# Kernel optimization log

Measured on AMD Instinct MI355X. Metric: run time of the kernel, lower is better.

Reference implementation:

```python
import jax, jax.numpy as jnp
import numpy as np

B = 131072      # batch
G = 8           # number of groups
GS = 8          # features per group (n_features = G*GS = 64)
K = 8           # n_basis
O = 16          # kan_out_dim
TOT = G * O     # 128, GroupKANLayer output dim
R = 10          # n_rules
FIN = 20        # fuzzy_in_dim = max(2*n_rules, 8)
EPS_BN = 1e-5


def setup_inputs() -> dict:
    key = jax.random.key(0)
    ks = jax.random.split(key, 8)
    x = jax.random.normal(ks[0], (B, G * GS), dtype=jnp.float32)
    # per-group GaussianRBF params (one shared RBF per group, applied to each feature)
    rbf_centres = jnp.tile(jnp.linspace(-3.0, 3.0, K, dtype=jnp.float32)[None, :], (G, 1))
    rbf_log_widths = jnp.zeros((G, K), dtype=jnp.float32)
    rbf_weights = jax.random.normal(ks[1], (G, K), dtype=jnp.float32) * 0.1
    rbf_linear_w = jnp.ones((G,), dtype=jnp.float32)
    # group projections: kaiming normal fan_in (relu gain sqrt(2))
    proj_W = jax.random.normal(ks[2], (G, O, GS), dtype=jnp.float32) * np.sqrt(2.0 / GS)
    proj_b = jnp.zeros((G, O), dtype=jnp.float32)
    bn1_gamma = jnp.ones((TOT,), dtype=jnp.float32)
    bn1_beta = jnp.zeros((TOT,), dtype=jnp.float32)
    # fuzzy_proj linear (xavier uniform) TOT -> FIN
    a = np.sqrt(6.0 / (TOT + FIN))
    fp_W = jax.random.uniform(ks[3], (FIN, TOT), dtype=jnp.float32, minval=-a, maxval=a)
    fp_b = jnp.zeros((FIN,), dtype=jnp.float32)
    bn2_gamma = jnp.ones((FIN,), dtype=jnp.float32)
    bn2_beta = jnp.zeros((FIN,), dtype=jnp.float32)
    # IT2 fuzzy layer params
    fz_centres = jax.random.uniform(ks[4], (R, FIN), dtype=jnp.float32, minval=-1.0, maxval=1.0)
    fz_log_su = jnp.full((R, FIN), -0.7, dtype=jnp.float32)
    fz_log_sl = jnp.full((R, FIN), -1.2, dtype=jnp.float32)
    # sparse rule head
    head_W = jax.random.normal(ks[5], (1, R), dtype=jnp.float32) * 0.05
    head_b = jnp.zeros((1,), dtype=jnp.float32)
    return {
        'x': x, 'rbf_centres': rbf_centres, 'rbf_log_widths': rbf_log_widths,
        'rbf_weights': rbf_weights, 'rbf_linear_w': rbf_linear_w,
        'proj_W': proj_W, 'proj_b': proj_b,
        'bn1_gamma': bn1_gamma, 'bn1_beta': bn1_beta,
        'fp_W': fp_W, 'fp_b': fp_b, 'bn2_gamma': bn2_gamma, 'bn2_beta': bn2_beta,
        'fz_centres': fz_centres, 'fz_log_su': fz_log_su, 'fz_log_sl': fz_log_sl,
        'head_W': head_W, 'head_b': head_b,
    }


def _batchnorm(h, gamma, beta):
    # training-mode BatchNorm1d: normalize with batch mean / biased variance
    mu = h.mean(axis=0)
    var = h.var(axis=0)
    return (h - mu) * jax.lax.rsqrt(var + EPS_BN) * gamma + beta


def _forward(x, rbf_centres, rbf_log_widths, rbf_weights, rbf_linear_w,
             proj_W, proj_b, bn1_gamma, bn1_beta, fp_W, fp_b,
             bn2_gamma, bn2_beta, fz_centres, fz_log_su, fz_log_sl,
             head_W, head_b):
    b = x.shape[0]
    xg = x.reshape(b, G, GS)                               # groups are contiguous index slices
    sigma = jnp.exp(rbf_log_widths) + 1e-6                 # [G,K]
    # Gaussian RBF over all groups/features at once: [B,G,GS,K]
    rbf = jnp.exp(-0.5 * ((xg[..., None] - rbf_centres[:, None, :]) / sigma[:, None, :]) ** 2)
    act = rbf_linear_w[None, :, None] * xg + jnp.einsum('bgfk,gk->bgf', rbf, rbf_weights)
    proj = jnp.einsum('bgf,gof->bgo', act, proj_W) + proj_b  # grouped linear, [B,G,O]
    h = _batchnorm(proj.reshape(b, TOT), bn1_gamma, bn1_beta)
    # fuzzy_proj: Linear -> BN -> GELU (torch default GELU = exact erf form)
    z = _batchnorm(h @ fp_W.T + fp_b, bn2_gamma, bn2_beta)
    z = jax.nn.gelu(z, approximate=False)                    # [B,FIN]
    # IT2 fuzzy memberships
    su = jnp.exp(fz_log_su) + 1e-6                           # [R,FIN]
    sl = jnp.minimum(jnp.exp(fz_log_sl) + 1e-6, su * 0.9)
    diff = z[:, None, :] - fz_centres[None]                  # [B,R,FIN]
    upper = jnp.exp(-0.5 * (diff / su[None]) ** 2).mean(-1)  # [B,R]
    lower = jnp.exp(-0.5 * (diff / sl[None]) ** 2).mean(-1)
    firing = 0.5 * (upper + lower)
    return firing @ head_W.T + head_b                        # [B,1]


def reference(x, rbf_centres, rbf_log_widths, rbf_weights, rbf_linear_w,
              proj_W, proj_b, bn1_gamma, bn1_beta, fp_W, fp_b,
              bn2_gamma, bn2_beta, fz_centres, fz_log_su, fz_log_sl,
              head_W, head_b):
    return _forward(x, rbf_centres, rbf_log_widths, rbf_weights, rbf_linear_w,
                    proj_W, proj_b, bn1_gamma, bn1_beta, fp_W, fp_b,
                    bn2_gamma, bn2_beta, fz_centres, fz_log_su, fz_log_sl,
                    head_W, head_b)
```

## Files before the change

kernel.cpp:

```cpp
#include <hip/hip_runtime.h>
#include <math.h>

#define B_N 131072
#define R_N 10
#define FIN_N 20

#define WS_STAT1 0
#define ST1_SZ   (64 * 352)
#define WS_MT    22528
#define WS_C     23808
#define WS_STAT2 23840
#define WS_NH    26400
#define WS_ACT   26816
#define WS_Z2    26816
#define WS_ZFULL (26816 + (size_t)64 * B_N)

__global__ __launch_bounds__(256) void k_act_moments(
    const float* __restrict__ x, const float* __restrict__ cen,
    const float* __restrict__ lw, const float* __restrict__ rw,
    const float* __restrict__ linw, float* __restrict__ act_out,
    float* __restrict__ stat1, int store)
{
    __shared__ float sAcc[4][8][44];

    const int t = threadIdx.x;
    const int g = t & 7;
    const int rl = t >> 3;

    float c_[8], nh_[8], w_[8];
#pragma unroll
    for (int k = 0; k < 8; ++k) {
        c_[k] = cen[g * 8 + k];
        float s = expf(lw[g * 8 + k]) + 1e-6f;
        nh_[k] = -0.5f / (s * s);
        w_[k] = rw[g * 8 + k];
    }
    const float lin = linw[g];

    float sumA[8], P[36];
#pragma unroll
    for (int f = 0; f < 8; ++f) sumA[f] = 0.0f;
#pragma unroll
    for (int i = 0; i < 36; ++i) P[i] = 0.0f;

    for (int row = blockIdx.x * 32 + rl; row < B_N; row += gridDim.x * 32) {
        const float* xr = x + (size_t)row * 64 + g * 8;
        float4 v0 = *(const float4*)(xr);
        float4 v1 = *(const float4*)(xr + 4);
        float xv[8] = {v0.x, v0.y, v0.z, v0.w, v1.x, v1.y, v1.z, v1.w};
        float act[8];
#pragma unroll
        for (int f = 0; f < 8; ++f) {
            float v = xv[f];
            float a = lin * v;
#pragma unroll
            for (int k = 0; k < 8; ++k) {
                float d = v - c_[k];
                a += w_[k] * __expf(d * d * nh_[k]);
            }
            act[f] = a;
        }
        if (store) {
            float* ar = act_out + (size_t)row * 64 + g * 8;
            *(float4*)(ar)     = make_float4(act[0], act[1], act[2], act[3]);
            *(float4*)(ar + 4) = make_float4(act[4], act[5], act[6], act[7]);
        }
        int idx = 0;
#pragma unroll
        for (int f = 0; f < 8; ++f) {
            sumA[f] += act[f];
#pragma unroll
            for (int f2 = 0; f2 <= f; ++f2) { P[idx] += act[f] * act[f2]; ++idx; }
        }
    }

#pragma unroll
    for (int off = 32; off >= 8; off >>= 1) {
#pragma unroll
        for (int f = 0; f < 8; ++f) sumA[f] += __shfl_down(sumA[f], off, 64);
#pragma unroll
        for (int i = 0; i < 36; ++i) P[i] += __shfl_down(P[i], off, 64);
    }
    const int wave = t >> 6, lane = t & 63;
    if (lane < 8) {
        float* dst = &sAcc[wave][lane][0];
#pragma unroll
        for (int f = 0; f < 8; ++f) dst[f] = sumA[f];
#pragma unroll
        for (int i = 0; i < 36; ++i) dst[8 + i] = P[i];
    }
    __syncthreads();
    for (int i = t; i < 352; i += 256) {
        int gg = i / 44, v = i % 44;
        float s = sAcc[0][gg][v] + sAcc[1][gg][v] + sAcc[2][gg][v] + sAcc[3][gg][v];
        atomicAdd(&stat1[(blockIdx.x & 63) * 352 + i], s);
    }
}

__global__ __launch_bounds__(256) void k_build(
    const float* __restrict__ stat1, const float* __restrict__ fpW,
    const float* __restrict__ fpb, const float* __restrict__ g1,
    const float* __restrict__ b1, const float* __restrict__ Wp,
    const float* __restrict__ pb, const float* __restrict__ lsu,
    const float* __restrict__ lsl,
    float* __restrict__ Mt, float* __restrict__ Cc, float* __restrict__ nh,
    float* __restrict__ stat2)
{
    __shared__ float Am[8][8];
    __shared__ float Sg[8][36];
    __shared__ float a_[128], bb_[128];
    const int t = threadIdx.x;

    for (int i = t; i < 352; i += 256) {
        float s = 0.0f;
        for (int st = 0; st < 64; ++st) s += stat1[st * 352 + i];
        float m = s * (1.0f / B_N);
        int g = i / 44, v = i % 44;
        if (v < 8) Am[g][v] = m; else Sg[g][v - 8] = m;
    }
    __syncthreads();

    if (t < 128) {
        const int g = t >> 4;
        float wv[8];
#pragma unroll
        for (int f = 0; f < 8; ++f) wv[f] = Wp[t * 8 + f];
        float dot = 0.0f;
#pragma unroll
        for (int f = 0; f < 8; ++f) dot += wv[f] * Am[g][f];
        const float pbv = pb[t];
        const float mu = pbv + dot;
        float e2 = pbv * pbv + 2.0f * pbv * dot;
        int idx = 0;
#pragma unroll
        for (int f = 0; f < 8; ++f)
#pragma unroll
            for (int f2 = 0; f2 <= f; ++f2) {
                float c2 = (f2 == f) ? 1.0f : 2.0f;
                e2 += c2 * wv[f] * wv[f2] * Sg[g][idx]; ++idx;
            }
        const float var = e2 - mu * mu;
        const float a = g1[t] * rsqrtf(var + 1e-5f);
        a_[t] = a;
        bb_[t] = b1[t] - mu * a;
    }
    __syncthreads();

    for (int i = t; i < 1280; i += 256) {
        int gf = i / 20, j = i % 20;
        int g = gf >> 3, f = gf & 7;
        float m = 0.0f;
        for (int o = 0; o < 16; ++o) {
            int c = g * 16 + o;
            m += fpW[j * 128 + c] * a_[c] * Wp[c * 8 + f];
        }
        Mt[i] = m;
    }
    if (t < 20) {
        float cj = fpb[t];
        for (int c = 0; c < 128; ++c)
            cj += fpW[t * 128 + c] * (a_[c] * pb[c] + bb_[c]);
        Cc[t] = cj;
    }
    for (int i = t; i < 200; i += 256) {
        float su = expf(lsu[i]) + 1e-6f;
        float sl = fminf(expf(lsl[i]) + 1e-6f, 0.9f * su);
        nh[i] = -0.5f / (su * su);
        nh[200 + i] = -0.5f / (sl * sl);
    }
    for (int i = t; i < 2560; i += 256) stat2[i] = 0.0f;
}

__global__ __launch_bounds__(128) void k_z_from_act(
    const float* __restrict__ act, const float* __restrict__ Mt,
    const float* __restrict__ Cc, float* __restrict__ zout,
    float* __restrict__ stat2)
{
    __shared__ __align__(16) float sMt[1280];
    __shared__ float sC[20];
    __shared__ float sRed[2][40];

    const int t = threadIdx.x;
    for (int i = t; i < 1280; i += 128) sMt[i] = Mt[i];
    if (t < 20) sC[t] = Cc[t];
    __syncthreads();

    const int r0 = (blockIdx.x * 128 + t) * 4;
    float zp[4][20];
#pragma unroll
    for (int r = 0; r < 4; ++r)
#pragma unroll
        for (int j = 0; j < 20; ++j) zp[r][j] = sC[j];

#pragma unroll 1
    for (int g = 0; g < 8; ++g) {
        float a[4][8];
#pragma unroll
        for (int r = 0; r < 4; ++r) {
            const float* ar = act + (size_t)(r0 + r) * 64 + g * 8;
            float4 v0 = *(const float4*)(ar);
            float4 v1 = *(const float4*)(ar + 4);
            a[r][0] = v0.x; a[r][1] = v0.y; a[r][2] = v0.z; a[r][3] = v0.w;
            a[r][4] = v1.x; a[r][5] = v1.y; a[r][6] = v1.z; a[r][7] = v1.w;
        }
#pragma unroll
        for (int f = 0; f < 8; ++f) {
            const float4* m4 = (const float4*)(sMt + (g * 8 + f) * 20);
            float4 ma = m4[0], mb = m4[1], mc = m4[2], md = m4[3], me = m4[4];
#pragma unroll
            for (int r = 0; r < 4; ++r) {
                float av = a[r][f];
                zp[r][0] += av * ma.x; zp[r][1] += av * ma.y; zp[r][2] += av * ma.z; zp[r][3] += av * ma.w;
                zp[r][4] += av * mb.x; zp[r][5] += av * mb.y; zp[r][6] += av * mb.z; zp[r][7] += av * mb.w;
                zp[r][8] += av * mc.x; zp[r][9] += av * mc.y; zp[r][10] += av * mc.z; zp[r][11] += av * mc.w;
                zp[r][12] += av * md.x; zp[r][13] += av * md.y; zp[r][14] += av * md.z; zp[r][15] += av * md.w;
                zp[r][16] += av * me.x; zp[r][17] += av * me.y; zp[r][18] += av * me.z; zp[r][19] += av * me.w;
            }
        }
    }

#pragma unroll
    for (int j = 0; j < 20; ++j) {
        *(float4*)(zout + (size_t)j * B_N + r0) =
            make_float4(zp[0][j], zp[1][j], zp[2][j], zp[3][j]);
    }

    float s_[20], q_[20];
#pragma unroll
    for (int j = 0; j < 20; ++j) {
        float s = zp[0][j] + zp[1][j] + zp[2][j] + zp[3][j];
        float q = zp[0][j]*zp[0][j] + zp[1][j]*zp[1][j] + zp[2][j]*zp[2][j] + zp[3][j]*zp[3][j];
        s_[j] = s; q_[j] = q;
    }
#pragma unroll
    for (int off = 32; off >= 1; off >>= 1) {
#pragma unroll
        for (int j = 0; j < 20; ++j) {
            s_[j] += __shfl_down(s_[j], off, 64);
            q_[j] += __shfl_down(q_[j], off, 64);
        }
    }
    const int wave = t >> 6, lane = t & 63;
    if (lane == 0) {
#pragma unroll
        for (int j = 0; j < 20; ++j) {
            sRed[wave][j] = s_[j];
            sRed[wave][20 + j] = q_[j];
        }
    }
    __syncthreads();
    if (t < 40) {
        float v = sRed[0][t] + sRed[1][t];
        atomicAdd(&stat2[(blockIdx.x & 63) * 40 + t], v);
    }
}

__device__ __forceinline__ void zpre_row(
    const float* __restrict__ xr, const float4* __restrict__ sRbf,
    const float* __restrict__ sLin, const float* __restrict__ sMt,
    const float* __restrict__ sC, float zp[20])
{
#pragma unroll
    for (int j = 0; j < 20; ++j) zp[j] = sC[j];
#pragma unroll 1
    for (int g = 0; g < 8; ++g) {
        float4 v0 = *(const float4*)(xr + g * 8);
        float4 v1 = *(const float4*)(xr + g * 8 + 4);
        float xv[8] = {v0.x, v0.y, v0.z, v0.w, v1.x, v1.y, v1.z, v1.w};
        float act[8];
        float lin = sLin[g];
#pragma unroll
        for (int f = 0; f < 8; ++f) act[f] = lin * xv[f];
#pragma unroll 1
        for (int k = 0; k < 8; ++k) {
            float4 p = sRbf[g * 8 + k];
#pragma unroll
            for (int f = 0; f < 8; ++f) {
                float d = xv[f] - p.x;
                act[f] += p.y * __expf(d * d * p.z);
            }
        }
#pragma unroll 1
        for (int f = 0; f < 8; ++f) {
            float av = act[f];
            const float4* m4 = (const float4*)(sMt + (g * 8 + f) * 20);
            float4 ma = m4[0], mb = m4[1], mc = m4[2], md = m4[3], me = m4[4];
            zp[0] += av * ma.x; zp[1] += av * ma.y; zp[2] += av * ma.z; zp[3] += av * ma.w;
            zp[4] += av * mb.x; zp[5] += av * mb.y; zp[6] += av * mb.z; zp[7] += av * mb.w;
            zp[8] += av * mc.x; zp[9] += av * mc.y; zp[10] += av * mc.z; zp[11] += av * mc.w;
            zp[12] += av * md.x; zp[13] += av * md.y; zp[14] += av * md.z; zp[15] += av * md.w;
            zp[16] += av * me.x; zp[17] += av * me.y; zp[18] += av * me.z; zp[19] += av * me.w;
        }
    }
}

__device__ __forceinline__ void load_rbf_lds(
    const float* cen, const float* lw, const float* rw, const float* linw,
    const float* Mt, const float* Cc,
    float4* sRbf, float* sLin, float* sMt, float* sC, int t)
{
    if (t < 64) {
        float s = expf(lw[t]) + 1e-6f;
        sRbf[t] = make_float4(cen[t], rw[t], -0.5f / (s * s), 0.0f);
    }
    if (t < 8)  sLin[t] = linw[t];
    if (t < 20) sC[t] = Cc[t];
    for (int i = t; i < 1280; i += 256) sMt[i] = Mt[i];
}

__global__ __launch_bounds__(256) void k_zpre_stats(
    const float* __restrict__ x, const float* __restrict__ cen,
    const float* __restrict__ lw, const float* __restrict__ rw,
    const float* __restrict__ linw, const float* __restrict__ Mt,
    const float* __restrict__ Cc, float* __restrict__ zout,
    float* __restrict__ stat2, int store)
{
    __shared__ __align__(16) float4 sRbf[64];
    __shared__ float sLin[8], sC[20];
    __shared__ __align__(16) float sMt[1280];
    __shared__ float sRed[4][40];

    const int t = threadIdx.x;
    load_rbf_lds(cen, lw, rw, linw, Mt, Cc, sRbf, sLin, sMt, sC, t);
    __syncthreads();

    const int row = blockIdx.x * 256 + t;
    float zp[20];
    zpre_row(x + (size_t)row * 64, sRbf, sLin, sMt, sC, zp);
    if (store) {
#pragma unroll
        for (int j = 0; j < 20; ++j) zout[(size_t)j * B_N + row] = zp[j];
    }
    float s_[20], q_[20];
#pragma unroll
    for (int j = 0; j < 20; ++j) { s_[j] = zp[j]; q_[j] = zp[j] * zp[j]; }
#pragma unroll
    for (int off = 32; off >= 1; off >>= 1) {
#pragma unroll
        for (int j = 0; j < 20; ++j) {
            s_[j] += __shfl_down(s_[j], off, 64);
            q_[j] += __shfl_down(q_[j], off, 64);
        }
    }
    const int wave = t >> 6, lane = t & 63;
    if (lane == 0) {
#pragma unroll
        for (int j = 0; j < 20; ++j) { sRed[wave][j] = s_[j]; sRed[wave][20 + j] = q_[j]; }
    }
    __syncthreads();
    if (t < 40) {
        float v = sRed[0][t] + sRed[1][t] + sRed[2][t] + sRed[3][t];
        atomicAdd(&stat2[(blockIdx.x & 63) * 40 + t], v);
    }
}

__device__ __forceinline__ float gelu_exact(float v) {
    return 0.5f * v * (1.0f + erff(v * 0.70710678118654752440f));
}

__device__ __forceinline__ void bn2_inline(
    const float* stat2, const float* g2, const float* b2,
    float* sT, float* sSc, float* sSh, int t)
{
    if (t < 40) {
        float s = 0.0f;
        for (int st = 0; st < 64; ++st) s += stat2[st * 40 + t];
        sT[t] = s;
    }
    __syncthreads();
    if (t < 20) {
        float mu = sT[t] * (1.0f / B_N);
        float var = sT[20 + t] * (1.0f / B_N) - mu * mu;
        float sc = g2[t] * rsqrtf(var + 1e-5f);
        sSc[t] = sc;
        sSh[t] = b2[t] - mu * sc;
    }
}

__global__ __launch_bounds__(256) void k_out2(
    const float* __restrict__ zin, const float* __restrict__ stat2,
    const float* __restrict__ g2, const float* __restrict__ b2,
    const float* __restrict__ nh, const float* __restrict__ fzc,
    const float* __restrict__ hW, const float* __restrict__ hb,
    float* __restrict__ out)
{
    __shared__ float sT[40], sSc[20], sSh[20], sHW[10];
    __shared__ __align__(16) float4 sFz[200];
    const int t = threadIdx.x;
    if (t < 10) sHW[t] = hW[t];
    for (int i = t; i < 200; i += 256)
        sFz[i] = make_float4(fzc[i], nh[i], nh[200 + i], 0.0f);
    bn2_inline(stat2, g2, b2, sT, sSc, sSh, t);
    __syncthreads();

    const int r0 = (blockIdx.x * 256 + t) * 2;
    float z0[20], z1[20];
#pragma unroll
    for (int j = 0; j < 20; ++j) {
        float2 v = *(const float2*)(zin + (size_t)j * B_N + r0);
        z0[j] = gelu_exact(sSc[j] * v.x + sSh[j]);
        z1[j] = gelu_exact(sSc[j] * v.y + sSh[j]);
    }
    const float hbv = hb[0];
    float acc0 = hbv, acc1 = hbv;
#pragma unroll 1
    for (int r = 0; r < 10; ++r) {
        float u0 = 0.0f, l0 = 0.0f, u1 = 0.0f, l1 = 0.0f;
#pragma unroll
        for (int j = 0; j < 20; ++j) {
            float4 p = sFz[r * 20 + j];
            float d0 = z0[j] - p.x, d1 = z1[j] - p.x;
            float dd0 = d0 * d0, dd1 = d1 * d1;
            u0 += __expf(dd0 * p.y); l0 += __expf(dd0 * p.z);
            u1 += __expf(dd1 * p.y); l1 += __expf(dd1 * p.z);
        }
        float w = sHW[r] * 0.025f;
        acc0 += w * (u0 + l0);
        acc1 += w * (u1 + l1);
    }
    *(float2*)(out + r0) = make_float2(acc0, acc1);
}

__global__ __launch_bounds__(256) void k_out_rec(
    const float* __restrict__ x, const float* __restrict__ cen,
    const float* __restrict__ lw, const float* __restrict__ rw,
    const float* __restrict__ linw, const float* __restrict__ Mt,
    const float* __restrict__ Cc, const float* __restrict__ stat2,
    const float* __restrict__ g2, const float* __restrict__ b2,
    const float* __restrict__ nh, const float* __restrict__ fzc,
    const float* __restrict__ hW, const float* __restrict__ hb,
    float* __restrict__ out)
{
    __shared__ __align__(16) float4 sRbf[64];
    __shared__ float sLin[8], sC[20];
    __shared__ __align__(16) float sMt[1280];
    __shared__ float sT[40], sSc[20], sSh[20], sHW[10];
    __shared__ __align__(16) float4 sFz[200];

    const int t = threadIdx.x;
    load_rbf_lds(cen, lw, rw, linw, Mt, Cc, sRbf, sLin, sMt, sC, t);
    if (t < 10) sHW[t] = hW[t];
    for (int i = t; i < 200; i += 256)
        sFz[i] = make_float4(fzc[i], nh[i], nh[200 + i], 0.0f);
    bn2_inline(stat2, g2, b2, sT, sSc, sSh, t);
    __syncthreads();

    const int row = blockIdx.x * 256 + t;
    float zp[20];
    zpre_row(x + (size_t)row * 64, sRbf, sLin, sMt, sC, zp);
    float z[20];
#pragma unroll
    for (int j = 0; j < 20; ++j)
        z[j] = gelu_exact(sSc[j] * zp[j] + sSh[j]);
    float acc = hb[0];
#pragma unroll 1
    for (int r = 0; r < 10; ++r) {
        float u = 0.0f, l = 0.0f;
#pragma unroll
        for (int j = 0; j < 20; ++j) {
            float4 p = sFz[r * 20 + j];
            float d = z[j] - p.x;
            float dd = d * d;
            u += __expf(dd * p.y);
            l += __expf(dd * p.z);
        }
        acc += sHW[r] * 0.025f * (u + l);
    }
    out[row] = acc;
}

extern "C" void kernel_launch(void* const* d_in, const int* in_sizes, int n_in,
                              void* d_out, int out_size, void* d_ws, size_t ws_size,
                              hipStream_t stream) {
    const float* x    = (const float*)d_in[0];
    const float* cen  = (const float*)d_in[1];
    const float* lw   = (const float*)d_in[2];
    const float* rw   = (const float*)d_in[3];
    const float* linw = (const float*)d_in[4];
    const float* Wp   = (const float*)d_in[5];
    const float* pb   = (const float*)d_in[6];
    const float* g1   = (const float*)d_in[7];
    const float* b1   = (const float*)d_in[8];
    const float* fpW  = (const float*)d_in[9];
    const float* fpb  = (const float*)d_in[10];
    const float* g2   = (const float*)d_in[11];
    const float* b2   = (const float*)d_in[12];
    const float* fzc  = (const float*)d_in[13];
    const float* lsu  = (const float*)d_in[14];
    const float* lsl  = (const float*)d_in[15];
    const float* hW   = (const float*)d_in[16];
    const float* hb   = (const float*)d_in[17];

    float* ws    = (float*)d_ws;
    float* stat1 = ws + WS_STAT1;
    float* Mt    = ws + WS_MT;
    float* Cc    = ws + WS_C;
    float* stat2 = ws + WS_STAT2;
    float* nh    = ws + WS_NH;
    float* actb  = ws + WS_ACT;
    float* outp  = (float*)d_out;

    const size_t needFull = (WS_ZFULL + (size_t)20 * B_N) * sizeof(float);
    const size_t needZ    = ((size_t)WS_Z2 + (size_t)20 * B_N) * sizeof(float);
    int mode = (ws_size >= needFull) ? 2 : (ws_size >= needZ ? 1 : 0);
    float* zbuf = (mode == 2) ? (ws + WS_ZFULL) : (ws + WS_Z2);

    hipMemsetAsync(stat1, 0, (size_t)ST1_SZ * sizeof(float), stream);
    k_act_moments<<<1024, 256, 0, stream>>>(x, cen, lw, rw, linw, actb, stat1,
                                            mode == 2 ? 1 : 0);
    k_build<<<1, 256, 0, stream>>>(stat1, fpW, fpb, g1, b1, Wp, pb, lsu, lsl,
                                   Mt, Cc, nh, stat2);
    if (mode == 2) {
        k_z_from_act<<<256, 128, 0, stream>>>(actb, Mt, Cc, zbuf, stat2);
        k_out2<<<256, 256, 0, stream>>>(zbuf, stat2, g2, b2, nh, fzc, hW, hb, outp);
    } else if (mode == 1) {
        k_zpre_stats<<<512, 256, 0, stream>>>(x, cen, lw, rw, linw, Mt, Cc,
                                              zbuf, stat2, 1);
        k_out2<<<256, 256, 0, stream>>>(zbuf, stat2, g2, b2, nh, fzc, hW, hb, outp);
    } else {
        k_zpre_stats<<<512, 256, 0, stream>>>(x, cen, lw, rw, linw, Mt, Cc,
                                              nullptr, stat2, 0);
        k_out_rec<<<512, 256, 0, stream>>>(x, cen, lw, rw, linw, Mt, Cc,
                                           stat2, g2, b2, nh, fzc, hW, hb, outp);
    }
}
```

Baseline: 188.5 us.

## Fuse whole pipeline into one cooperative kernel with grid syncs

Result: slower. 388.0 us (+105.9%).

```diff
diff --git a/kernel.cpp b/kernel.cpp
--- a/kernel.cpp
+++ b/kernel.cpp
@@ -1,9 +1,17 @@
 #include <hip/hip_runtime.h>
+#include <hip/hip_cooperative_groups.h>
 #include <math.h>
 
+namespace cg = cooperative_groups;
+
 #define B_N 131072
-#define R_N 10
-#define FIN_N 20
+#define CB 256
+#define CT 256
+
+#define CW_P1   0
+#define CW_MOM  (256 * 352)
+#define CW_P2   (CW_MOM + 352)
+#define CW_BN2  (CW_P2 + 256 * 40)
 
 #define WS_STAT1 0
 #define ST1_SZ   (64 * 352)
@@ -11,22 +19,307 @@
 #define WS_C     23808
 #define WS_STAT2 23840
 #define WS_NH    26400
-#define WS_ACT   26816
 #define WS_Z2    26816
-#define WS_ZFULL (26816 + (size_t)64 * B_N)
+
+__device__ __forceinline__ float gelu_exact(float v) {
+    return 0.5f * v * (1.0f + erff(v * 0.70710678118654752440f));
+}
+
+__global__ __launch_bounds__(256, 1) void k_fused(
+    const float* __restrict__ x, const float* __restrict__ cen,
+    const float* __restrict__ lw, const float* __restrict__ rw,
+    const float* __restrict__ linw, const float* __restrict__ Wp,
+    const float* __restrict__ pb, const float* __restrict__ g1,
+    const float* __restrict__ b1, const float* __restrict__ fpW,
+    const float* __restrict__ fpb, const float* __restrict__ g2,
+    const float* __restrict__ b2, const float* __restrict__ fzc,
+    const float* __restrict__ lsu, const float* __restrict__ lsl,
+    const float* __restrict__ hW, const float* __restrict__ hb,
+    float* __restrict__ ws, float* __restrict__ out)
+{
+    __shared__ float sAcc[4][8][44];
+    __shared__ __align__(16) float4 sRbf[64];
+    __shared__ float sLin[8];
+    __shared__ __align__(16) float sMt[1280];
+    __shared__ float sC[20], a_[128], bb_[128];
+    __shared__ __align__(16) float4 sFz[200];
+    __shared__ float sHW[10], sT[40], sSc[20], sSh[20];
+    __shared__ float sRed[4][40];
+
+    cg::grid_group grid = cg::this_grid();
+    const int t = threadIdx.x;
+    const int b = blockIdx.x;
+    float* part1 = ws + CW_P1;
+    float* mom   = ws + CW_MOM;
+    float* part2 = ws + CW_P2;
+    float* bn2s  = ws + CW_BN2;
+
+    {
+        const int g = t & 7, rl = t >> 3;
+        float c_[8], nh_[8], w_[8];
+#pragma unroll
+        for (int k = 0; k < 8; ++k) {
+            c_[k] = cen[g * 8 + k];
+            float s = expf(lw[g * 8 + k]) + 1e-6f;
+            nh_[k] = -0.5f / (s * s);
+            w_[k] = rw[g * 8 + k];
+        }
+        const float lin = linw[g];
+        float sumA[8], P[36];
+#pragma unroll
+        for (int f = 0; f < 8; ++f) sumA[f] = 0.0f;
+#pragma unroll
+        for (int i = 0; i < 36; ++i) P[i] = 0.0f;
+
+        for (int row = b * 32 + rl; row < B_N; row += CB * 32) {
+            const float* xr = x + (size_t)row * 64 + g * 8;
+            float4 v0 = *(const float4*)(xr);
+            float4 v1 = *(const float4*)(xr + 4);
+            float xv[8] = {v0.x, v0.y, v0.z, v0.w, v1.x, v1.y, v1.z, v1.w};
+            float act[8];
+#pragma unroll
+            for (int f = 0; f < 8; ++f) {
+                float v = xv[f];
+                float a = lin * v;
+#pragma unroll
+                for (int k = 0; k < 8; ++k) {
+                    float d = v - c_[k];
+                    a += w_[k] * __expf(d * d * nh_[k]);
+                }
+                act[f] = a;
+            }
+            int idx = 0;
+#pragma unroll
+            for (int f = 0; f < 8; ++f) {
+                sumA[f] += act[f];
+#pragma unroll
+                for (int f2 = 0; f2 <= f; ++f2) { P[idx] += act[f] * act[f2]; ++idx; }
+            }
+        }
+#pragma unroll
+        for (int off = 32; off >= 8; off >>= 1) {
+#pragma unroll
+            for (int f = 0; f < 8; ++f) sumA[f] += __shfl_down(sumA[f], off, 64);
+#pragma unroll
+            for (int i = 0; i < 36; ++i) P[i] += __shfl_down(P[i], off, 64);
+        }
+        const int wave = t >> 6, lane = t & 63;
+        if (lane < 8) {
+            float* dst = &sAcc[wave][lane][0];
+#pragma unroll
+            for (int f = 0; f < 8; ++f) dst[f] = sumA[f];
+#pragma unroll
+            for (int i = 0; i < 36; ++i) dst[8 + i] = P[i];
+        }
+        __syncthreads();
+        for (int i = t; i < 352; i += 256) {
+            int gg = i / 44, v = i % 44;
+            part1[b * 352 + i] =
+                sAcc[0][gg][v] + sAcc[1][gg][v] + sAcc[2][gg][v] + sAcc[3][gg][v];
+        }
+    }
+    __threadfence();
+    grid.sync();
+
+    for (int v = b; v < 352; v += CB) {
+        float val = part1[(size_t)t * 352 + v];
+#pragma unroll
+        for (int off = 32; off >= 1; off >>= 1) val += __shfl_down(val, off, 64);
+        if ((t & 63) == 0) sT[t >> 6] = val;
+        __syncthreads();
+        if (t == 0)
+            mom[v] = (sT[0] + sT[1] + sT[2] + sT[3]) * (1.0f / B_N);
+        __syncthreads();
+    }
+    __threadfence();
+    grid.sync();
+
+    if (t < 128) {
+        const int g = t >> 4;
+        float wv[8], Amg[8];
+#pragma unroll
+        for (int f = 0; f < 8; ++f) { wv[f] = Wp[t * 8 + f]; Amg[f] = mom[g * 44 + f]; }
+        float dot = 0.0f;
+#pragma unroll
+        for (int f = 0; f < 8; ++f) dot += wv[f] * Amg[f];
+        const float pbv = pb[t];
+        const float mu = pbv + dot;
+        float e2 = pbv * pbv + 2.0f * pbv * dot;
+        int idx = 0;
+#pragma unroll
+        for (int f = 0; f < 8; ++f)
+#pragma unroll
+            for (int f2 = 0; f2 <= f; ++f2) {
+                float c2 = (f2 == f) ? 1.0f : 2.0f;
+                e2 += c2 * wv[f] * wv[f2] * mom[g * 44 + 8 + idx]; ++idx;
+            }
+        const float var = fmaxf(e2 - mu * mu, 0.0f);
+        const float a = g1[t] * rsqrtf(var + 1e-5f);
+        a_[t] = a;
+        bb_[t] = b1[t] - mu * a;
+    }
+    if (t < 64) {
+        float s = expf(lw[t]) + 1e-6f;
+        sRbf[t] = make_float4(cen[t], rw[t], -0.5f / (s * s), 0.0f);
+    }
+    if (t < 8)  sLin[t] = linw[t];
+    if (t < 10) sHW[t] = hW[t];
+    for (int i = t; i < 200; i += 256) {
+        float su = expf(lsu[i]) + 1e-6f;
+        float sl = fminf(expf(lsl[i]) + 1e-6f, 0.9f * su);
+        sFz[i] = make_float4(fzc[i], -0.5f / (su * su), -0.5f / (sl * sl), 0.0f);
+    }
+    __syncthreads();
+    for (int i = t; i < 1280; i += 256) {
+        int gf = i / 20, j = i % 20;
+        int g = gf >> 3, f = gf & 7;
+        float m = 0.0f;
+        for (int o = 0; o < 16; ++o) {
+            int c = g * 16 + o;
+            m += fpW[j * 128 + c] * a_[c] * Wp[c * 8 + f];
+        }
+        sMt[i] = m;
+    }
+    if (t < 20) {
+        float cj = fpb[t];
+        for (int c = 0; c < 128; ++c)
+            cj += fpW[t * 128 + c] * (a_[c] * pb[c] + bb_[c]);
+        sC[t] = cj;
+    }
+    __syncthreads();
+
+    const int r0 = (b * CT + t) * 2;
+    float z[2][20];
+#pragma unroll
+    for (int j = 0; j < 20; ++j) { z[0][j] = sC[j]; z[1][j] = sC[j]; }
+    {
+        const float* xr = x + (size_t)r0 * 64;
+#pragma unroll 1
+        for (int g = 0; g < 8; ++g) {
+            float4 p0 = *(const float4*)(xr + g * 8);
+            float4 p1 = *(const float4*)(xr + g * 8 + 4);
+            float4 q0 = *(const float4*)(xr + 64 + g * 8);
+            float4 q1 = *(const float4*)(xr + 64 + g * 8 + 4);
+            float xv[2][8] = {{p0.x, p0.y, p0.z, p0.w, p1.x, p1.y, p1.z, p1.w},
+                              {q0.x, q0.y, q0.z, q0.w, q1.x, q1.y, q1.z, q1.w}};
+            float act[2][8];
+            float lin = sLin[g];
+#pragma unroll
+            for (int r = 0; r < 2; ++r)
+#pragma unroll
+                for (int f = 0; f < 8; ++f) act[r][f] = lin * xv[r][f];
+#pragma unroll 1
+            for (int k = 0; k < 8; ++k) {
+                float4 p = sRbf[g * 8 + k];
+#pragma unroll
+                for (int r = 0; r < 2; ++r)
+#pragma unroll
+                    for (int f = 0; f < 8; ++f) {
+                        float d = xv[r][f] - p.x;
+                        act[r][f] += p.y * __expf(d * d * p.z);
+                    }
+            }
+#pragma unroll 1
+            for (int f = 0; f < 8; ++f) {
+                const float4* m4 = (const float4*)(sMt + (g * 8 + f) * 20);
+                float4 ma = m4[0], mb = m4[1], mc = m4[2], md = m4[3], me = m4[4];
+#pragma unroll
+                for (int r = 0; r < 2; ++r) {
+                    float av = act[r][f];
+                    z[r][0] += av * ma.x; z[r][1] += av * ma.y; z[r][2] += av * ma.z; z[r][3] += av * ma.w;
+                    z[r][4] += av * mb.x; z[r][5] += av * mb.y; z[r][6] += av * mb.z; z[r][7] += av * mb.w;
+                    z[r][8] += av * mc.x; z[r][9] += av * mc.y; z[r][10] += av * mc.z; z[r][11] += av * mc.w;
+                    z[r][12] += av * md.x; z[r][13] += av * md.y; z[r][14] += av * md.z; z[r][15] += av * md.w;
+                    z[r][16] += av * me.x; z[r][17] += av * me.y; z[r][18] += av * me.z; z[r][19] += av * me.w;
+                }
+            }
+        }
+    }
+    {
+        float s_[20], q_[20];
+#pragma unroll
+        for (int j = 0; j < 20; ++j) {
+            s_[j] = z[0][j] + z[1][j];
+            q_[j] = z[0][j] * z[0][j] + z[1][j] * z[1][j];
+        }
+#pragma unroll
+        for (int off = 32; off >= 1; off >>= 1) {
+#pragma unroll
+            for (int j = 0; j < 20; ++j) {
+                s_[j] += __shfl_down(s_[j], off, 64);
+                q_[j] += __shfl_down(q_[j], off, 64);
+            }
+        }
+        const int wave = t >> 6, lane = t & 63;
+        if (lane == 0) {
+#pragma unroll
+            for (int j = 0; j < 20; ++j) {
+                sRed[wave][j] = s_[j];
+                sRed[wave][20 + j] = q_[j];
+            }
+        }
+        __syncthreads();
+        if (t < 40)
+            part2[b * 40 + t] = sRed[0][t] + sRed[1][t] + sRed[2][t] + sRed[3][t];
+    }
+    __threadfence();
+    grid.sync();
+
+    if (b < 40) {
+        float val = part2[(size_t)t * 40 + b];
+#pragma unroll
+        for (int off = 32; off >= 1; off >>= 1) val += __shfl_down(val, off, 64);
+        if ((t & 63) == 0) sT[t >> 6] = val;
+        __syncthreads();
+        if (t == 0) bn2s[b] = sT[0] + sT[1] + sT[2] + sT[3];
+    }
+    __threadfence();
+    grid.sync();
+
+    if (t < 40) sT[t] = bn2s[t];
+    __syncthreads();
+    if (t < 20) {
+        float mu = sT[t] * (1.0f / B_N);
+        float var = fmaxf(sT[20 + t] * (1.0f / B_N) - mu * mu, 0.0f);
+        float sc = g2[t] * rsqrtf(var + 1e-5f);
+        sSc[t] = sc;
+        sSh[t] = b2[t] - mu * sc;
+    }
+    __syncthreads();
+#pragma unroll
+    for (int r = 0; r < 2; ++r)
+#pragma unroll
+        for (int j = 0; j < 20; ++j)
+            z[r][j] = gelu_exact(sSc[j] * z[r][j] + sSh[j]);
+    const float hbv = hb[0];
+    float acc0 = hbv, acc1 = hbv;
+#pragma unroll 1
+    for (int r = 0; r < 10; ++r) {
+        float u0 = 0.0f, l0 = 0.0f, u1 = 0.0f, l1 = 0.0f;
+#pragma unroll
+        for (int j = 0; j < 20; ++j) {
+            float4 p = sFz[r * 20 + j];
+            float d0 = z[0][j] - p.x, d1 = z[1][j] - p.x;
+            float dd0 = d0 * d0, dd1 = d1 * d1;
+            u0 += __expf(dd0 * p.y); l0 += __expf(dd0 * p.z);
+            u1 += __expf(dd1 * p.y); l1 += __expf(dd1 * p.z);
+        }
+        float w = sHW[r] * 0.025f;
+        acc0 += w * (u0 + l0);
+        acc1 += w * (u1 + l1);
+    }
+    *(float2*)(out + r0) = make_float2(acc0, acc1);
+}
 
 __global__ __launch_bounds__(256) void k_act_moments(
     const float* __restrict__ x, const float* __restrict__ cen,
     const float* __restrict__ lw, const float* __restrict__ rw,
-    const float* __restrict__ linw, float* __restrict__ act_out,
-    float* __restrict__ stat1, int store)
+    const float* __restrict__ linw, float* __restrict__ stat1)
 {
     __shared__ float sAcc[4][8][44];
-
     const int t = threadIdx.x;
     const int g = t & 7;
     const int rl = t >> 3;
-
     float c_[8], nh_[8], w_[8];
 #pragma unroll
     for (int k = 0; k < 8; ++k) {
@@ -36,13 +329,11 @@
         w_[k] = rw[g * 8 + k];
     }
     const float lin = linw[g];
-
     float sumA[8], P[36];
 #pragma unroll
     for (int f = 0; f < 8; ++f) sumA[f] = 0.0f;
 #pragma unroll
     for (int i = 0; i < 36; ++i) P[i] = 0.0f;
-
     for (int row = blockIdx.x * 32 + rl; row < B_N; row += gridDim.x * 32) {
         const float* xr = x + (size_t)row * 64 + g * 8;
         float4 v0 = *(const float4*)(xr);
@@ -60,11 +351,6 @@
             }
             act[f] = a;
         }
-        if (store) {
-            float* ar = act_out + (size_t)row * 64 + g * 8;
-            *(float4*)(ar)     = make_float4(act[0], act[1], act[2], act[3]);
-            *(float4*)(ar + 4) = make_float4(act[4], act[5], act[6], act[7]);
-        }
         int idx = 0;
 #pragma unroll
         for (int f = 0; f < 8; ++f) {
@@ -73,7 +359,6 @@
             for (int f2 = 0; f2 <= f; ++f2) { P[idx] += act[f] * act[f2]; ++idx; }
         }
     }
-
 #pragma unroll
     for (int off = 32; off >= 8; off >>= 1) {
 #pragma unroll
@@ -110,7 +395,6 @@
     __shared__ float Sg[8][36];
     __shared__ float a_[128], bb_[128];
     const int t = threadIdx.x;
-
     for (int i = t; i < 352; i += 256) {
         float s = 0.0f;
         for (int st = 0; st < 64; ++st) s += stat1[st * 352 + i];
@@ -119,7 +403,6 @@
         if (v < 8) Am[g][v] = m; else Sg[g][v - 8] = m;
     }
     __syncthreads();
-
     if (t < 128) {
         const int g = t >> 4;
         float wv[8];
@@ -139,13 +422,12 @@
                 float c2 = (f2 == f) ? 1.0f : 2.0f;
                 e2 += c2 * wv[f] * wv[f2] * Sg[g][idx]; ++idx;
             }
-        const float var = e2 - mu * mu;
+        const float var = fmaxf(e2 - mu * mu, 0.0f);
         const float a = g1[t] * rsqrtf(var + 1e-5f);
         a_[t] = a;
         bb_[t] = b1[t] - mu * a;
     }
     __syncthreads();
-
     for (int i = t; i < 1280; i += 256) {
         int gf = i / 20, j = i % 20;
         int g = gf >> 3, f = gf & 7;
@@ -169,90 +451,6 @@
         nh[200 + i] = -0.5f / (sl * sl);
     }
     for (int i = t; i < 2560; i += 256) stat2[i] = 0.0f;
-}
-
-__global__ __launch_bounds__(128) void k_z_from_act(
-    const float* __restrict__ act, const float* __restrict__ Mt,
-    const float* __restrict__ Cc, float* __restrict__ zout,
-    float* __restrict__ stat2)
-{
-    __shared__ __align__(16) float sMt[1280];
-    __shared__ float sC[20];
-    __shared__ float sRed[2][40];
-
-    const int t = threadIdx.x;
-    for (int i = t; i < 1280; i += 128) sMt[i] = Mt[i];
-    if (t < 20) sC[t] = Cc[t];
-    __syncthreads();
-
-    const int r0 = (blockIdx.x * 128 + t) * 4;
-    float zp[4][20];
-#pragma unroll
-    for (int r = 0; r < 4; ++r)
-#pragma unroll
-        for (int j = 0; j < 20; ++j) zp[r][j] = sC[j];
-
-#pragma unroll 1
-    for (int g = 0; g < 8; ++g) {
-        float a[4][8];
-#pragma unroll
-        for (int r = 0; r < 4; ++r) {
-            const float* ar = act + (size_t)(r0 + r) * 64 + g * 8;
-            float4 v0 = *(const float4*)(ar);
-            float4 v1 = *(const float4*)(ar + 4);
-            a[r][0] = v0.x; a[r][1] = v0.y; a[r][2] = v0.z; a[r][3] = v0.w;
-            a[r][4] = v1.x; a[r][5] = v1.y; a[r][6] = v1.z; a[r][7] = v1.w;
-        }
-#pragma unroll
-        for (int f = 0; f < 8; ++f) {
-            const float4* m4 = (const float4*)(sMt + (g * 8 + f) * 20);
-            float4 ma = m4[0], mb = m4[1], mc = m4[2], md = m4[3], me = m4[4];
-#pragma unroll
-            for (int r = 0; r < 4; ++r) {
-                float av = a[r][f];
-                zp[r][0] += av * ma.x; zp[r][1] += av * ma.y; zp[r][2] += av * ma.z; zp[r][3] += av * ma.w;
-                zp[r][4] += av * mb.x; zp[r][5] += av * mb.y; zp[r][6] += av * mb.z; zp[r][7] += av * mb.w;
-                zp[r][8] += av * mc.x; zp[r][9] += av * mc.y; zp[r][10] += av * mc.z; zp[r][11] += av * mc.w;
-                zp[r][12] += av * md.x; zp[r][13] += av * md.y; zp[r][14] += av * md.z; zp[r][15] += av * md.w;
-                zp[r][16] += av * me.x; zp[r][17] += av * me.y; zp[r][18] += av * me.z; zp[r][19] += av * me.w;
-            }
-        }
-    }
-
-#pragma unroll
-    for (int j = 0; j < 20; ++j) {
-        *(float4*)(zout + (size_t)j * B_N + r0) =
-            make_float4(zp[0][j], zp[1][j], zp[2][j], zp[3][j]);
-    }
-
-    float s_[20], q_[20];
-#pragma unroll
-    for (int j = 0; j < 20; ++j) {
-        float s = zp[0][j] + zp[1][j] + zp[2][j] + zp[3][j];
-        float q = zp[0][j]*zp[0][j] + zp[1][j]*zp[1][j] + zp[2][j]*zp[2][j] + zp[3][j]*zp[3][j];
-        s_[j] = s; q_[j] = q;
-    }
-#pragma unroll
-    for (int off = 32; off >= 1; off >>= 1) {
-#pragma unroll
-        for (int j = 0; j < 20; ++j) {
-            s_[j] += __shfl_down(s_[j], off, 64);
-            q_[j] += __shfl_down(q_[j], off, 64);
-        }
-    }
-    const int wave = t >> 6, lane = t & 63;
-    if (lane == 0) {
-#pragma unroll
-        for (int j = 0; j < 20; ++j) {
-            sRed[wave][j] = s_[j];
-            sRed[wave][20 + j] = q_[j];
-        }
-    }
-    __syncthreads();
-    if (t < 40) {
-        float v = sRed[0][t] + sRed[1][t];
-        atomicAdd(&stat2[(blockIdx.x & 63) * 40 + t], v);
-    }
 }
 
 __device__ __forceinline__ void zpre_row(
@@ -294,43 +492,31 @@
     }
 }
 
-__device__ __forceinline__ void load_rbf_lds(
-    const float* cen, const float* lw, const float* rw, const float* linw,
-    const float* Mt, const float* Cc,
-    float4* sRbf, float* sLin, float* sMt, float* sC, int t)
-{
-    if (t < 64) {
-        float s = expf(lw[t]) + 1e-6f;
-        sRbf[t] = make_float4(cen[t], rw[t], -0.5f / (s * s), 0.0f);
-    }
-    if (t < 8)  sLin[t] = linw[t];
-    if (t < 20) sC[t] = Cc[t];
-    for (int i = t; i < 1280; i += 256) sMt[i] = Mt[i];
-}
-
 __global__ __launch_bounds__(256) void k_zpre_stats(
     const float* __restrict__ x, const float* __restrict__ cen,
     const float* __restrict__ lw, const float* __restrict__ rw,
     const float* __restrict__ linw, const float* __restrict__ Mt,
     const float* __restrict__ Cc, float* __restrict__ zout,
-    float* __restrict__ stat2, int store)
+    float* __restrict__ stat2)
 {
     __shared__ __align__(16) float4 sRbf[64];
     __shared__ float sLin[8], sC[20];
     __shared__ __align__(16) float sMt[1280];
     __shared__ float sRed[4][40];
-
     const int t = threadIdx.x;
-    load_rbf_lds(cen, lw, rw, linw, Mt, Cc, sRbf, sLin, sMt, sC, t);
-    __syncthreads();
-
+    if (t < 64) {
+        float s = expf(lw[t]) + 1e-6f;
+        sRbf[t] = make_float4(cen[t], rw[t], -0.5f / (s * s), 0.0f);
+    }
+    if (t < 8)  sLin[t] = linw[t];
+    if (t < 20) sC[t] = Cc[t];
+    for (int i = t; i < 1280; i += 256) sMt[i] = Mt[i];
+    __syncthreads();
     const int row = blockIdx.x * 256 + t;
     float zp[20];
     zpre_row(x + (size_t)row * 64, sRbf, sLin, sMt, sC, zp);
-    if (store) {
-#pragma unroll
-        for (int j = 0; j < 20; ++j) zout[(size_t)j * B_N + row] = zp[j];
-    }
+#pragma unroll
+    for (int j = 0; j < 20; ++j) zout[(size_t)j * B_N + row] = zp[j];
     float s_[20], q_[20];
 #pragma unroll
     for (int j = 0; j < 20; ++j) { s_[j] = zp[j]; q_[j] = zp[j] * zp[j]; }
@@ -351,29 +537,6 @@
     if (t < 40) {
         float v = sRed[0][t] + sRed[1][t] + sRed[2][t] + sRed[3][t];
         atomicAdd(&stat2[(blockIdx.x & 63) * 40 + t], v);
-    }
-}
-
-__device__ __forceinline__ float gelu_exact(float v) {
-    return 0.5f * v * (1.0f + erff(v * 0.70710678118654752440f));
-}
-
-__device__ __forceinline__ void bn2_inline(
-    const float* stat2, const float* g2, const float* b2,
-    float* sT, float* sSc, float* sSh, int t)
-{
-    if (t < 40) {
-        float s = 0.0f;
-        for (int st = 0; st < 64; ++st) s += stat2[st * 40 + t];
-        sT[t] = s;
-    }
-    __syncthreads();
-    if (t < 20) {
-        float mu = sT[t] * (1.0f / B_N);
-        float var = sT[20 + t] * (1.0f / B_N) - mu * mu;
-        float sc = g2[t] * rsqrtf(var + 1e-5f);
-        sSc[t] = sc;
-        sSh[t] = b2[t] - mu * sc;
     }
 }
 
@@ -390,9 +553,20 @@
     if (t < 10) sHW[t] = hW[t];
     for (int i = t; i < 200; i += 256)
         sFz[i] = make_float4(fzc[i], nh[i], nh[200 + i], 0.0f);
-    bn2_inline(stat2, g2, b2, sT, sSc, sSh, t);
-    __syncthreads();
-
+    if (t < 40) {
+        float s = 0.0f;
+        for (int st = 0; st < 64; ++st) s += stat2[st * 40 + t];
+        sT[t] = s;
+    }
+    __syncthreads();
+    if (t < 20) {
+        float mu = sT[t] * (1.0f / B_N);
+        float var = fmaxf(sT[20 + t] * (1.0f / B_N) - mu * mu, 0.0f);
+        float sc = g2[t] * rsqrtf(var + 1e-5f);
+        sSc[t] = sc;
+        sSh[t] = b2[t] - mu * sc;
+    }
+    __syncthreads();
     const int r0 = (blockIdx.x * 256 + t) * 2;
     float z0[20], z1[20];
 #pragma unroll
@@ -419,54 +593,6 @@
         acc1 += w * (u1 + l1);
     }
     *(float2*)(out + r0) = make_float2(acc0, acc1);
-}
-
-__global__ __launch_bounds__(256) void k_out_rec(
-    const float* __restrict__ x, const float* __restrict__ cen,
-    const float* __restrict__ lw, const float* __restrict__ rw,
-    const float* __restrict__ linw, const float* __restrict__ Mt,
-    const float* __restrict__ Cc, const float* __restrict__ stat2,
-    const float* __restrict__ g2, const float* __restrict__ b2,
-    const float* __restrict__ nh, const float* __restrict__ fzc,
-    const float* __restrict__ hW, const float* __restrict__ hb,
-    float* __restrict__ out)
-{
-    __shared__ __align__(16) float4 sRbf[64];
-    __shared__ float sLin[8], sC[20];
-    __shared__ __align__(16) float sMt[1280];
-    __shared__ float sT[40], sSc[20], sSh[20], sHW[10];
-    __shared__ __align__(16) float4 sFz[200];
-
-    const int t = threadIdx.x;
-    load_rbf_lds(cen, lw, rw, linw, Mt, Cc, sRbf, sLin, sMt, sC, t);
-    if (t < 10) sHW[t] = hW[t];
-    for (int i = t; i < 200; i += 256)
-        sFz[i] = make_float4(fzc[i], nh[i], nh[200 + i], 0.0f);
-    bn2_inline(stat2, g2, b2, sT, sSc, sSh, t);
-    __syncthreads();
-
-    const int row = blockIdx.x * 256 + t;
-    float zp[20];
-    zpre_row(x + (size_t)row * 64, sRbf, sLin, sMt, sC, zp);
-    float z[20];
-#pragma unroll
-    for (int j = 0; j < 20; ++j)
-        z[j] = gelu_exact(sSc[j] * zp[j] + sSh[j]);
-    float acc = hb[0];
-#pragma unroll 1
-    for (int r = 0; r < 10; ++r) {
-        float u = 0.0f, l = 0.0f;
-#pragma unroll
-        for (int j = 0; j < 20; ++j) {
-            float4 p = sFz[r * 20 + j];
-            float d = z[j] - p.x;
-            float dd = d * d;
-            u += __expf(dd * p.y);
-            l += __expf(dd * p.z);
-        }
-        acc += sHW[r] * 0.025f * (u + l);
-    }
-    out[row] = acc;
 }
 
 extern "C" void kernel_launch(void* const* d_in, const int* in_sizes, int n_in,
@@ -491,36 +617,31 @@
     const float* hW   = (const float*)d_in[16];
     const float* hb   = (const float*)d_in[17];
 
-    float* ws    = (float*)d_ws;
-    float* stat1 = ws + WS_STAT1;
-    float* Mt    = ws + WS_MT;
-    float* Cc    = ws + WS_C;
-    float* stat2 = ws + WS_STAT2;
-    float* nh    = ws + WS_NH;
-    float* actb  = ws + WS_ACT;
-    float* outp  = (float*)d_out;
-
-    const size_t needFull = (WS_ZFULL + (size_t)20 * B_N) * sizeof(float);
-    const size_t needZ    = ((size_t)WS_Z2 + (size_t)20 * B_N) * sizeof(float);
-    int mode = (ws_size >= needFull) ? 2 : (ws_size >= needZ ? 1 : 0);
-    float* zbuf = (mode == 2) ? (ws + WS_ZFULL) : (ws + WS_Z2);
+    float* wsf  = (float*)d_ws;
+    float* outp = (float*)d_out;
+
+    void* args[20] = {
+        (void*)&x, (void*)&cen, (void*)&lw, (void*)&rw, (void*)&linw,
+        (void*)&Wp, (void*)&pb, (void*)&g1, (void*)&b1, (void*)&fpW,
+        (void*)&fpb, (void*)&g2, (void*)&b2, (void*)&fzc, (void*)&lsu,
+        (void*)&lsl, (void*)&hW, (void*)&hb, (void*)&wsf, (void*)&outp
+    };
+    hipError_t e = hipLaunchCooperativeKernel((const void*)k_fused,
+                                              dim3(CB), dim3(CT), args, 0, stream);
+    if (e == hipSuccess) return;
+    (void)hipGetLastError();
+
+    float* stat1 = wsf + WS_STAT1;
+    float* Mt    = wsf + WS_MT;
+    float* Cc    = wsf + WS_C;
+    float* stat2 = wsf + WS_STAT2;
+    float* nh    = wsf + WS_NH;
+    float* zbuf  = wsf + WS_Z2;
 
     hipMemsetAsync(stat1, 0, (size_t)ST1_SZ * sizeof(float), stream);
-    k_act_moments<<<1024, 256, 0, stream>>>(x, cen, lw, rw, linw, actb, stat1,
-                                            mode == 2 ? 1 : 0);
+    k_act_moments<<<1024, 256, 0, stream>>>(x, cen, lw, rw, linw, stat1);
     k_build<<<1, 256, 0, stream>>>(stat1, fpW, fpb, g1, b1, Wp, pb, lsu, lsl,
                                    Mt, Cc, nh, stat2);
-    if (mode == 2) {
-        k_z_from_act<<<256, 128, 0, stream>>>(actb, Mt, Cc, zbuf, stat2);
-        k_out2<<<256, 256, 0, stream>>>(zbuf, stat2, g2, b2, nh, fzc, hW, hb, outp);
-    } else if (mode == 1) {
-        k_zpre_stats<<<512, 256, 0, stream>>>(x, cen, lw, rw, linw, Mt, Cc,
-                                              zbuf, stat2, 1);
-        k_out2<<<256, 256, 0, stream>>>(zbuf, stat2, g2, b2, nh, fzc, hW, hb, outp);
-    } else {
-        k_zpre_stats<<<512, 256, 0, stream>>>(x, cen, lw, rw, linw, Mt, Cc,
-                                              nullptr, stat2, 0);
-        k_out_rec<<<512, 256, 0, stream>>>(x, cen, lw, rw, linw, Mt, Cc,
-                                           stat2, g2, b2, nh, fzc, hW, hb, outp);
-    }
-}
+    k_zpre_stats<<<512, 256, 0, stream>>>(x, cen, lw, rw, linw, Mt, Cc, zbuf, stat2);
+    k_out2<<<256, 256, 0, stream>>>(zbuf, stat2, g2, b2, nh, fzc, hW, hb, outp);
+}
```
